# Performance work log

Hardware: AMD Instinct MI355X
Metric: run time of the kernel (lower is better)

The kernel has to match this reference:

```python
import jax, jax.numpy as jnp
import numpy as np

N = 10000        # nodes
E = 640000       # edges (before self-loops)
IN = 128         # in_channels
HID = 32         # hidden_channels
HEADS = 4
HC = HID * HEADS # 128
OUT = 40         # out_channels
NEG_SLOPE = 0.2  # PyG GATConv default


def setup_inputs() -> dict:
    key = jax.random.key(0)
    ks = jax.random.split(key, 12)
    g = lambda k, shape: (jax.random.normal(k, shape, jnp.float32) * 0.1)
    return {
        "x": jax.random.normal(ks[0], (N, IN), jnp.float32),
        "edge_index": jax.random.randint(ks[1], (2, E), 0, N, dtype=jnp.int32),
        # conv1: in -> HID per head, HEADS heads, concat
        "W1": g(ks[2], (IN, HEADS * HID)),
        "a_src1": g(ks[3], (HEADS, HID)),
        "a_dst1": g(ks[4], (HEADS, HID)),
        "b1": jnp.zeros((HEADS * HID,), jnp.float32),
        # conv2: HC -> HC, 1 head
        "W2": g(ks[5], (HC, HC)),
        "a_src2": g(ks[6], (1, HC)),
        "a_dst2": g(ks[7], (1, HC)),
        "b2": jnp.zeros((HC,), jnp.float32),
        # final linear head
        "Wlin": g(ks[8], (HC, OUT)),
        "blin": jnp.zeros((OUT,), jnp.float32),
    }


def _gat_layer(x, W, a_src, a_dst, b, src, dst, heads, n):
    """PyG-style GATConv: gather -> edge attention -> segment softmax -> scatter."""
    d = W.shape[1] // heads
    h = (x @ W).reshape(n, heads, d)                       # [N, H, d]
    asrc = jnp.einsum('nhd,hd->nh', h, a_src)              # [N, H]
    adst = jnp.einsum('nhd,hd->nh', h, a_dst)
    e = jax.nn.leaky_relu(asrc[src] + adst[dst], NEG_SLOPE)  # [E, H]
    m = jax.ops.segment_max(e, dst, num_segments=n)          # per-dst max (stable softmax)
    p = jnp.exp(e - m[dst])
    z = jax.ops.segment_sum(p, dst, num_segments=n)
    alpha = p / (z[dst] + 1e-16)                             # [E, H]
    out = jax.ops.segment_sum(h[src] * alpha[:, :, None], dst, num_segments=n)
    return out.reshape(n, heads * d) + b


def reference(x, edge_index, W1, a_src1, a_dst1, b1, W2, a_src2, a_dst2, b2, Wlin, blin):
    n = x.shape[0]
    loop = jnp.arange(n, dtype=edge_index.dtype)           # add_self_loops=True
    src = jnp.concatenate([edge_index[0], loop])
    dst = jnp.concatenate([edge_index[1], loop])
    # eval mode: dropout is identity
    h1 = jax.nn.elu(_gat_layer(x, W1, a_src1, a_dst1, b1, src, dst, HEADS, n))
    h2 = jax.nn.elu(_gat_layer(h1, W2, a_src2, a_dst2, b2, src, dst, 1, n))
    return h2 @ Wlin + blin
```

## Files before the change

kernel.cpp:

```cpp
#include <hip/hip_runtime.h>
#include <hip/hip_bf16.h>

#define KSUB 8
#define SUBCAP 32
#define CAP 256

using bf16x8 = __attribute__((ext_vector_type(8))) short;
using f32x4  = __attribute__((ext_vector_type(4))) float;

static __device__ __forceinline__ short f2b(float f) {
    __hip_bfloat16 h = __float2bfloat16(f);
    return *reinterpret_cast<short*>(&h);
}
static __device__ __forceinline__ float blo(unsigned u) { return __uint_as_float(u << 16); }
static __device__ __forceinline__ float bhi(unsigned u) { return __uint_as_float(u & 0xffff0000u); }

__device__ __forceinline__ int slot8(int idx, const int* pref) {
    int k = 0;
#pragma unroll
    for (int j = 1; j < KSUB; j++) k += (idx >= pref[j]);
    return k * SUBCAP + (idx - pref[k]);
}

__global__ __launch_bounds__(256) void build_csr_prep(
        const int* __restrict__ srcArr, const int* __restrict__ dstArr,
        int E, int N, int* __restrict__ deg2, unsigned short* __restrict__ csr,
        const float* __restrict__ W1, const float* __restrict__ W2,
        short* __restrict__ Wt1, short* __restrict__ Wt2, int NCB) {
    __shared__ float t[32][33];
    int tid = threadIdx.x;
    if ((int)blockIdx.x >= NCB) {
        int pb = blockIdx.x - NCB;
        int which = pb >> 4;
        int tile = pb & 15;
        int bi = tile >> 2, bj = tile & 3;
        const float* W = which ? W2 : W1;
        short* Wt = which ? Wt2 : Wt1;
        int tx = tid & 31, ty = tid >> 5;
#pragma unroll
        for (int i = 0; i < 4; i++) {
            int r = bi * 32 + ty + 8 * i;
            t[ty + 8 * i][tx] = W[r * 128 + bj * 32 + tx];
        }
        __syncthreads();
#pragma unroll
        for (int i = 0; i < 4; i++) {
            int j = bj * 32 + ty + 8 * i;
            Wt[j * 128 + bi * 32 + tx] = f2b(t[tx][ty + 8 * i]);
        }
        return;
    }
    int k_sub = blockIdx.x & (KSUB - 1);
    int Etot = E + N;
    int base = blockIdx.x * 1024 + tid;
#pragma unroll
    for (int k = 0; k < 4; k++) {
        int i = base + k * 256;
        if (i < Etot) {
            int s, d;
            if (i < E) { s = srcArr[i]; d = dstArr[i]; }
            else       { s = d = i - E; }
            int p = atomicAdd(&deg2[d * KSUB + k_sub], 1);
            if (p < SUBCAP) csr[d * CAP + k_sub * SUBCAP + p] = (unsigned short)s;
        }
    }
}

template <int H>
__global__ __launch_bounds__(256) void gemm_mfma(const float* __restrict__ x,
                        const short* __restrict__ Wt,
                        const float* __restrict__ a_src, const float* __restrict__ a_dst,
                        __hip_bfloat16* __restrict__ hwb, float* __restrict__ asrc,
                        float* __restrict__ adst, int N) {
    int wave = (blockIdx.x * 256 + threadIdx.x) >> 6;
    int lane = threadIdx.x & 63;
    int n0 = wave * 16;
    if (n0 >= N) return;
    int m = lane & 15, q = lane >> 4;
    int row = n0 + m;
    bf16x8 afrag[4];
    const float* xr = x + (size_t)row * 128 + q * 8;
#pragma unroll
    for (int kt = 0; kt < 4; kt++) {
        float4 v0 = *(const float4*)(xr + kt * 32);
        float4 v1 = *(const float4*)(xr + kt * 32 + 4);
        bf16x8 f;
        f[0] = f2b(v0.x); f[1] = f2b(v0.y); f[2] = f2b(v0.z); f[3] = f2b(v0.w);
        f[4] = f2b(v1.x); f[5] = f2b(v1.y); f[6] = f2b(v1.z); f[7] = f2b(v1.w);
        afrag[kt] = f;
    }
    float vs[4] = {0.f,0.f,0.f,0.f}, vd[4] = {0.f,0.f,0.f,0.f};
#pragma unroll
    for (int ct = 0; ct < 8; ct++) {
        f32x4 acc = {0.f, 0.f, 0.f, 0.f};
        const short* wrow = Wt + (ct * 16 + m) * 128 + q * 8;
#pragma unroll
        for (int kt = 0; kt < 4; kt++) {
            bf16x8 bfrag = *(const bf16x8*)(wrow + kt * 32);
            acc = __builtin_amdgcn_mfma_f32_16x16x32_bf16(afrag[kt], bfrag, acc, 0, 0, 0);
        }
        int col = ct * 16 + m;
        float asv = a_src[col], adv = a_dst[col];
#pragma unroll
        for (int r = 0; r < 4; r++) {
            int rr = n0 + q * 4 + r;
            hwb[rr * 128 + col] = __float2bfloat16(acc[r]);
            vs[r] += acc[r] * asv;
            vd[r] += acc[r] * adv;
        }
        if (H == 4 && (ct & 1) == 1) {
#pragma unroll
            for (int r = 0; r < 4; r++) {
                float a = vs[r], d = vd[r];
                for (int off = 8; off >= 1; off >>= 1) {
                    a += __shfl_xor(a, off); d += __shfl_xor(d, off);
                }
                if (m == 0) {
                    int rr = n0 + q * 4 + r;
                    asrc[rr * 4 + (ct >> 1)] = a;
                    adst[rr * 4 + (ct >> 1)] = d;
                }
                vs[r] = 0.f; vd[r] = 0.f;
            }
        }
    }
    if (H == 1) {
#pragma unroll
        for (int r = 0; r < 4; r++) {
            float a = vs[r], d = vd[r];
            for (int off = 8; off >= 1; off >>= 1) {
                a += __shfl_xor(a, off); d += __shfl_xor(d, off);
            }
            if (m == 0) {
                int rr = n0 + q * 4 + r;
                asrc[rr] = a;
                adst[rr] = d;
            }
        }
    }
}

__global__ __launch_bounds__(64) void agg4(const __hip_bfloat16* __restrict__ hw,
                     const float* __restrict__ asrc, const float* __restrict__ adst,
                     const int* __restrict__ deg2, const unsigned short* __restrict__ csr_src,
                     const float* __restrict__ b, float* __restrict__ y, int N) {
    int n = blockIdx.x;
    int t = threadIdx.x;
    int er = t >> 4;
    int cg = t & 15;
    int hcol = cg >> 2;
    const int4* dp = (const int4*)&deg2[n * KSUB];
    int4 ca = dp[0], cb2 = dp[1];
    int pref[KSUB];
    int cnts[KSUB] = { min(ca.x,SUBCAP), min(ca.y,SUBCAP), min(ca.z,SUBCAP), min(ca.w,SUBCAP),
                       min(cb2.x,SUBCAP), min(cb2.y,SUBCAP), min(cb2.z,SUBCAP), min(cb2.w,SUBCAP) };
    pref[0] = 0;
#pragma unroll
    for (int k = 1; k < KSUB; k++) pref[k] = pref[k-1] + cnts[k-1];
    int deg = pref[KSUB-1] + cnts[KSUB-1];
    const uint4* hw4 = (const uint4*)hw;
    __shared__ float pe[128 * 4];
    __shared__ int se[128];
    float4 adl = *(const float4*)&adst[n * 4];
    float acc[8] = {0.f,0.f,0.f,0.f,0.f,0.f,0.f,0.f};
    float z0 = 0.f, z1 = 0.f, z2 = 0.f, z3 = 0.f;
    for (int base = 0; base < deg; base += 128) {
        int cnt = min(128, deg - base);
        __syncthreads();
#pragma unroll
        for (int rep = 0; rep < 2; rep++) {
            int idx = t + 64 * rep;
            if (idx < cnt) {
                int s = (int)csr_src[n * CAP + slot8(base + idx, pref)];
                se[idx] = s;
                float4 av = *(const float4*)&asrc[s * 4];
                float e0 = av.x + adl.x, e1 = av.y + adl.y;
                float e2 = av.z + adl.z, e3 = av.w + adl.w;
                e0 = e0 > 0.f ? e0 : 0.2f * e0;
                e1 = e1 > 0.f ? e1 : 0.2f * e1;
                e2 = e2 > 0.f ? e2 : 0.2f * e2;
                e3 = e3 > 0.f ? e3 : 0.2f * e3;
                float p0 = __expf(e0), p1 = __expf(e1), p2 = __expf(e2), p3 = __expf(e3);
                pe[idx * 4 + 0] = p0; pe[idx * 4 + 1] = p1;
                pe[idx * 4 + 2] = p2; pe[idx * 4 + 3] = p3;
                z0 += p0; z1 += p1; z2 += p2; z3 += p3;
            }
        }
        __syncthreads();
        for (int c = er; c < cnt; c += 4) {
            int s = se[c];
            float p = pe[c * 4 + hcol];
            uint4 v = hw4[s * 16 + cg];
            acc[0] += p * blo(v.x); acc[1] += p * bhi(v.x);
            acc[2] += p * blo(v.y); acc[3] += p * bhi(v.y);
            acc[4] += p * blo(v.z); acc[5] += p * bhi(v.z);
            acc[6] += p * blo(v.w); acc[7] += p * bhi(v.w);
        }
    }
#pragma unroll
    for (int i = 0; i < 8; i++) {
        acc[i] += __shfl_xor(acc[i], 16);
        acc[i] += __shfl_xor(acc[i], 32);
    }
    for (int off = 32; off >= 1; off >>= 1) {
        z0 += __shfl_xor(z0, off); z1 += __shfl_xor(z1, off);
        z2 += __shfl_xor(z2, off); z3 += __shfl_xor(z3, off);
    }
    float z = (hcol == 0) ? z0 : (hcol == 1) ? z1 : (hcol == 2) ? z2 : z3;
    float inv = 1.f / (z + 1e-16f);
    int col = cg * 8 + er * 2;
    float2 bb = *(const float2*)&b[col];
    float r0 = acc[er * 2]     * inv + bb.x;
    float r1 = acc[er * 2 + 1] * inv + bb.y;
    r0 = r0 > 0.f ? r0 : (__expf(r0) - 1.0f);
    r1 = r1 > 0.f ? r1 : (__expf(r1) - 1.0f);
    *(float2*)&y[n * 128 + col] = make_float2(r0, r1);
}

__global__ __launch_bounds__(64) void agg1_lin(const __hip_bfloat16* __restrict__ hw,
                         const float* __restrict__ asrc, const float* __restrict__ adst,
                         const int* __restrict__ deg2, const unsigned short* __restrict__ csr_src,
                         const float* __restrict__ b, const float* __restrict__ Wl,
                         const float* __restrict__ bl, float* __restrict__ out,
                         int N, int OUTC) {
    int n = blockIdx.x;
    int t = threadIdx.x;
    int er = t >> 4;
    int cg = t & 15;
    const int4* dp = (const int4*)&deg2[n * KSUB];
    int4 ca = dp[0], cb2 = dp[1];
    int pref[KSUB];
    int cnts[KSUB] = { min(ca.x,SUBCAP), min(ca.y,SUBCAP), min(ca.z,SUBCAP), min(ca.w,SUBCAP),
                       min(cb2.x,SUBCAP), min(cb2.y,SUBCAP), min(cb2.z,SUBCAP), min(cb2.w,SUBCAP) };
    pref[0] = 0;
#pragma unroll
    for (int k = 1; k < KSUB; k++) pref[k] = pref[k-1] + cnts[k-1];
    int deg = pref[KSUB-1] + cnts[KSUB-1];
    const uint4* hw4 = (const uint4*)hw;
    __shared__ float pe[128];
    __shared__ int se[128];
    __shared__ float yrow[128];
    float adl = adst[n];
    float acc[8] = {0.f,0.f,0.f,0.f,0.f,0.f,0.f,0.f};
    float zp = 0.f;
    for (int base = 0; base < deg; base += 128) {
        int cnt = min(128, deg - base);
        __syncthreads();
#pragma unroll
        for (int rep = 0; rep < 2; rep++) {
            int idx = t + 64 * rep;
            if (idx < cnt) {
                int s = (int)csr_src[n * CAP + slot8(base + idx, pref)];
                se[idx] = s;
                float e = asrc[s] + adl;
                e = e > 0.f ? e : 0.2f * e;
                float p = __expf(e);
                pe[idx] = p;
                zp += p;
            }
        }
        __syncthreads();
        for (int c = er; c < cnt; c += 4) {
            int s = se[c];
            float p = pe[c];
            uint4 v = hw4[s * 16 + cg];
            acc[0] += p * blo(v.x); acc[1] += p * bhi(v.x);
            acc[2] += p * blo(v.y); acc[3] += p * bhi(v.y);
            acc[4] += p * blo(v.z); acc[5] += p * bhi(v.z);
            acc[6] += p * blo(v.w); acc[7] += p * bhi(v.w);
        }
    }
#pragma unroll
    for (int i = 0; i < 8; i++) {
        acc[i] += __shfl_xor(acc[i], 16);
        acc[i] += __shfl_xor(acc[i], 32);
    }
    for (int off = 32; off >= 1; off >>= 1) zp += __shfl_xor(zp, off);
    float inv = 1.f / (zp + 1e-16f);
    int col = cg * 8 + er * 2;
    float2 bb = *(const float2*)&b[col];
    float r0 = acc[er * 2]     * inv + bb.x;
    float r1 = acc[er * 2 + 1] * inv + bb.y;
    r0 = r0 > 0.f ? r0 : (__expf(r0) - 1.0f);
    r1 = r1 > 0.f ? r1 : (__expf(r1) - 1.0f);
    yrow[col] = r0; yrow[col + 1] = r1;
    __syncthreads();
    if (t < OUTC) {
        float a = bl[t];
        for (int k = 0; k < 128; k++) a += yrow[k] * Wl[k * OUTC + t];
        out[n * OUTC + t] = a;
    }
}

extern "C" void kernel_launch(void* const* d_in, const int* in_sizes, int n_in,
                              void* d_out, int out_size, void* d_ws, size_t ws_size,
                              hipStream_t stream) {
    const float* x       = (const float*)d_in[0];
    const int*   ei      = (const int*)d_in[1];
    const float* W1      = (const float*)d_in[2];
    const float* a_src1  = (const float*)d_in[3];
    const float* a_dst1  = (const float*)d_in[4];
    const float* b1      = (const float*)d_in[5];
    const float* W2      = (const float*)d_in[6];
    const float* a_src2  = (const float*)d_in[7];
    const float* a_dst2  = (const float*)d_in[8];
    const float* b2      = (const float*)d_in[9];
    const float* Wlin    = (const float*)d_in[10];
    const float* blin    = (const float*)d_in[11];
    float* out = (float*)d_out;

    const int N = in_sizes[0] / 128;
    const int E = in_sizes[1] / 2;
    const int OUTC = in_sizes[10] / 128;
    const int Etot = E + N;
    const int* src = ei;
    const int* dst = ei + E;
    const int NCB = (Etot + 1023) / 1024;
    const int NGB = (N / 16 + 3) / 4;

    char* w = (char*)d_ws;
    size_t off = 0;
    auto alloc = [&](size_t bytes) -> char* {
        char* p = w + off;
        off += (bytes + 255) & ~(size_t)255;
        return p;
    };
    int*             deg2  = (int*)alloc((size_t)N * KSUB * 4);
    unsigned short*  csr   = (unsigned short*)alloc((size_t)N * CAP * 2);
    __hip_bfloat16*  hwb   = (__hip_bfloat16*)alloc((size_t)N * 128 * 2);
    float*           bufY  = (float*)alloc((size_t)N * 128 * 4);
    short*           Wt1   = (short*)alloc((size_t)128 * 128 * 2);
    short*           Wt2   = (short*)alloc((size_t)128 * 128 * 2);
    float*           asrc1 = (float*)alloc((size_t)N * 4 * 4);
    float*           adst1 = (float*)alloc((size_t)N * 4 * 4);
    float*           asrc2 = (float*)alloc((size_t)N * 4);
    float*           adst2 = (float*)alloc((size_t)N * 4);
    (void)ws_size;

    hipMemsetAsync(deg2, 0, (size_t)N * KSUB * 4, stream);
    build_csr_prep<<<NCB + 32, 256, 0, stream>>>(src, dst, E, N, deg2, csr,
                                                 W1, W2, Wt1, Wt2, NCB);

    gemm_mfma<4><<<NGB, 256, 0, stream>>>(x, Wt1, a_src1, a_dst1, hwb, asrc1, adst1, N);
    agg4<<<N, 64, 0, stream>>>(hwb, asrc1, adst1, deg2, csr, b1, bufY, N);

    gemm_mfma<1><<<NGB, 256, 0, stream>>>(bufY, Wt2, a_src2, a_dst2, hwb, asrc2, adst2, N);
    agg1_lin<<<N, 64, 0, stream>>>(hwb, asrc2, adst2, deg2, csr, b2, Wlin, blin, out, N, OUTC);
}
```

Before: 175.7 us.

## Fuse layer-2 linear transform and attention scores into layer-1 aggregation kernel

Layer-1 aggregation now keeps each node's ELU output row in shared memory and multiplies it by the bf16 transposed W2 per block, writing hw2 as bf16 along with the layer-2 source and destination attention scores. This removes the second MFMA GEMM launch and the fp32 intermediate buffer write and read. The cost is scalar FMAs instead of MFMA for the 128x128 product, with each block reading all of W2, which stays cache-resident.

New measurement: 196.2 us. +11.7%, slower.

```diff
diff --git a/kernel.cpp b/kernel.cpp
--- a/kernel.cpp
+++ b/kernel.cpp
@@ -66,8 +66,7 @@
     }
 }
 
-template <int H>
-__global__ __launch_bounds__(256) void gemm_mfma(const float* __restrict__ x,
+__global__ __launch_bounds__(256) void gemm_mfma4(const float* __restrict__ x,
                         const short* __restrict__ Wt,
                         const float* __restrict__ a_src, const float* __restrict__ a_dst,
                         __hip_bfloat16* __restrict__ hwb, float* __restrict__ asrc,
@@ -108,7 +107,7 @@
             vs[r] += acc[r] * asv;
             vd[r] += acc[r] * adv;
         }
-        if (H == 4 && (ct & 1) == 1) {
+        if ((ct & 1) == 1) {
 #pragma unroll
             for (int r = 0; r < 4; r++) {
                 float a = vs[r], d = vd[r];
@@ -124,26 +123,15 @@
             }
         }
     }
-    if (H == 1) {
-#pragma unroll
-        for (int r = 0; r < 4; r++) {
-            float a = vs[r], d = vd[r];
-            for (int off = 8; off >= 1; off >>= 1) {
-                a += __shfl_xor(a, off); d += __shfl_xor(d, off);
-            }
-            if (m == 0) {
-                int rr = n0 + q * 4 + r;
-                asrc[rr] = a;
-                adst[rr] = d;
-            }
-        }
-    }
-}
-
-__global__ __launch_bounds__(64) void agg4(const __hip_bfloat16* __restrict__ hw,
+}
+
+__global__ __launch_bounds__(64) void agg4_g2(const __hip_bfloat16* __restrict__ hw,
                      const float* __restrict__ asrc, const float* __restrict__ adst,
                      const int* __restrict__ deg2, const unsigned short* __restrict__ csr_src,
-                     const float* __restrict__ b, float* __restrict__ y, int N) {
+                     const float* __restrict__ b, const short* __restrict__ Wt2,
+                     const float* __restrict__ as2, const float* __restrict__ ad2,
+                     __hip_bfloat16* __restrict__ hwb2, float* __restrict__ asrc2,
+                     float* __restrict__ adst2, int N) {
     int n = blockIdx.x;
     int t = threadIdx.x;
     int er = t >> 4;
@@ -161,6 +149,7 @@
     const uint4* hw4 = (const uint4*)hw;
     __shared__ float pe[128 * 4];
     __shared__ int se[128];
+    __shared__ float yrow[128];
     float4 adl = *(const float4*)&adst[n * 4];
     float acc[8] = {0.f,0.f,0.f,0.f,0.f,0.f,0.f,0.f};
     float z0 = 0.f, z1 = 0.f, z2 = 0.f, z3 = 0.f;
@@ -214,7 +203,31 @@
     float r1 = acc[er * 2 + 1] * inv + bb.y;
     r0 = r0 > 0.f ? r0 : (__expf(r0) - 1.0f);
     r1 = r1 > 0.f ? r1 : (__expf(r1) - 1.0f);
-    *(float2*)&y[n * 128 + col] = make_float2(r0, r1);
+    yrow[col] = r0; yrow[col + 1] = r1;
+    __syncthreads();
+    int co0 = col, co1 = col + 1;
+    const uint4* w0 = (const uint4*)(Wt2 + (size_t)co0 * 128);
+    const uint4* w1 = (const uint4*)(Wt2 + (size_t)co1 * 128);
+    float a0 = 0.f, a1 = 0.f;
+#pragma unroll
+    for (int kk = 0; kk < 16; kk++) {
+        uint4 wa = w0[kk];
+        uint4 wb = w1[kk];
+        const float* yk = &yrow[kk * 8];
+        a0 += yk[0]*blo(wa.x) + yk[1]*bhi(wa.x) + yk[2]*blo(wa.y) + yk[3]*bhi(wa.y)
+            + yk[4]*blo(wa.z) + yk[5]*bhi(wa.z) + yk[6]*blo(wa.w) + yk[7]*bhi(wa.w);
+        a1 += yk[0]*blo(wb.x) + yk[1]*bhi(wb.x) + yk[2]*blo(wb.y) + yk[3]*bhi(wb.y)
+            + yk[4]*blo(wb.z) + yk[5]*bhi(wb.z) + yk[6]*blo(wb.w) + yk[7]*bhi(wb.w);
+    }
+    hwb2[n * 128 + co0] = __float2bfloat16(a0);
+    hwb2[n * 128 + co1] = __float2bfloat16(a1);
+    float ps = a0 * as2[co0] + a1 * as2[co1];
+    float pd = a0 * ad2[co0] + a1 * ad2[co1];
+    for (int off = 32; off >= 1; off >>= 1) {
+        ps += __shfl_xor(ps, off);
+        pd += __shfl_xor(pd, off);
+    }
+    if (t == 0) { asrc2[n] = ps; adst2[n] = pd; }
 }
 
 __global__ __launch_bounds__(64) void agg1_lin(const __hip_bfloat16* __restrict__ hw,
@@ -328,7 +341,7 @@
     int*             deg2  = (int*)alloc((size_t)N * KSUB * 4);
     unsigned short*  csr   = (unsigned short*)alloc((size_t)N * CAP * 2);
     __hip_bfloat16*  hwb   = (__hip_bfloat16*)alloc((size_t)N * 128 * 2);
-    float*           bufY  = (float*)alloc((size_t)N * 128 * 4);
+    __hip_bfloat16*  hwb2  = (__hip_bfloat16*)alloc((size_t)N * 128 * 2);
     short*           Wt1   = (short*)alloc((size_t)128 * 128 * 2);
     short*           Wt2   = (short*)alloc((size_t)128 * 128 * 2);
     float*           asrc1 = (float*)alloc((size_t)N * 4 * 4);
@@ -341,9 +354,11 @@
     build_csr_prep<<<NCB + 32, 256, 0, stream>>>(src, dst, E, N, deg2, csr,
                                                  W1, W2, Wt1, Wt2, NCB);
 
-    gemm_mfma<4><<<NGB, 256, 0, stream>>>(x, Wt1, a_src1, a_dst1, hwb, asrc1, adst1, N);
-    agg4<<<N, 64, 0, stream>>>(hwb, asrc1, adst1, deg2, csr, b1, bufY, N);
-
-    gemm_mfma<1><<<NGB, 256, 0, stream>>>(bufY, Wt2, a_src2, a_dst2, hwb, asrc2, adst2, N);
-    agg1_lin<<<N, 64, 0, stream>>>(hwb, asrc2, adst2, deg2, csr, b2, Wlin, blin, out, N, OUTC);
-}
+    gemm_mfma4<<<NGB, 256, 0, stream>>>(x, Wt1, a_src1, a_dst1, hwb, asrc1, adst1, N);
+
+    agg4_g2<<<N, 64, 0, stream>>>(hwb, asrc1, adst1, deg2, csr, b1,
+                                  Wt2, a_src2, a_dst2, hwb2, asrc2, adst2, N);
+
+    agg1_lin<<<N, 64, 0, stream>>>(hwb2, asrc2, adst2, deg2, csr, b2, Wlin, blin,
+                                   out, N, OUTC);
+}
```
